# Optimization experiments

Hardware: AMD Instinct MI355X
Metric: run time of the kernel (lower is better)

Reference implementation:

```python
import jax, jax.numpy as jnp
import numpy as np

N_NODES = 50000
N_EDGES = 800000
D = 128        # input_dim == output_dim
D_EDGE = 64    # edge_attr_size
Z_DIM = 2 * D + D_EDGE  # 320


def setup_inputs() -> dict:
    key = jax.random.key(0)
    k1, k2, k3, k4, k5 = jax.random.split(key, 5)
    x = jax.random.normal(k1, (N_NODES, D), dtype=jnp.float32)
    edge_index = jax.random.randint(k2, (2, N_EDGES), 0, N_NODES, dtype=jnp.int64)
    edge_attr = jax.random.normal(k3, (N_EDGES, D_EDGE), dtype=jnp.float32)
    scale = 1.0 / np.sqrt(Z_DIM)
    W_f = jax.random.normal(k4, (Z_DIM, D), dtype=jnp.float32) * scale
    W_s = jax.random.normal(k5, (Z_DIM, D), dtype=jnp.float32) * scale
    b_f = jnp.zeros((D,), dtype=jnp.float32)
    b_s = jnp.zeros((D,), dtype=jnp.float32)
    return {"x": x, "edge_index": edge_index, "edge_attr": edge_attr,
            "W_f": W_f, "b_f": b_f, "W_s": W_s, "b_s": b_s}


def reference(x, edge_index, edge_attr, W_f, b_f, W_s, b_s):
    # Dropout(p=0.0) is identity in inference.
    src = edge_index[0]  # j (message source)
    dst = edge_index[1]  # i (message target)
    # z_e = [x_i, x_j, e_ij]  -> [E, 2D + D_edge]
    z = jnp.concatenate([x[dst], x[src], edge_attr], axis=-1)
    # CGConv message: sigmoid(lin_f(z)) * softplus(lin_s(z))
    msg = jax.nn.sigmoid(z @ W_f + b_f) * jax.nn.softplus(z @ W_s + b_s)
    # scatter-add aggregation + residual
    out = jax.ops.segment_sum(msg, dst, num_segments=x.shape[0]) + x
    # use_activation=True -> ReLU
    return jax.nn.relu(out)
```

## Files before the change

kernel.cpp:

```cpp
#include <hip/hip_runtime.h>
#include <hip/hip_bf16.h>

#define E_TOTAL   800000
#define NN        50000
#define DD        128
#define DE        64
#define ZDIM      320
#define KE        192
#define MT        64
#define NBS       196

typedef short bf16x8 __attribute__((ext_vector_type(8)));
typedef float f32x4  __attribute__((ext_vector_type(4)));

__device__ __forceinline__ unsigned short f2bf(float f) {
    union { float f; unsigned int u; } v; v.f = f;
    unsigned int u = v.u;
    return (unsigned short)((u + 0x7fffu + ((u >> 16) & 1u)) >> 16);
}

__device__ __forceinline__ float bf2f(unsigned short h) {
    union { unsigned u; float f; } v; v.u = ((unsigned)h) << 16; return v.f;
}

__device__ __forceinline__ unsigned pkbf2(float a, float b) {
    __hip_bfloat162 h = __float22bfloat162_rn(make_float2(a, b));
    unsigned u; __builtin_memcpy(&u, &h, 4); return u;
}

__device__ __forceinline__ uint2 pkbf4(float4 v) {
    uint2 r; r.x = pkbf2(v.x, v.y); r.y = pkbf2(v.z, v.w); return r;
}

__device__ __forceinline__ float fast_rcp(float x) {
#if __has_builtin(__builtin_amdgcn_rcpf)
    return __builtin_amdgcn_rcpf(x);
#else
    return 1.0f / x;
#endif
}


__global__ void scan_part(const int* __restrict__ counts, int* __restrict__ partial) {
    __shared__ int red[256];
    int t = threadIdx.x, k = blockIdx.x * 256 + t;
    red[t] = (k < NN) ? counts[k] : 0;
    __syncthreads();
    for (int d = 128; d > 0; d >>= 1) {
        if (t < d) red[t] += red[t + d];
        __syncthreads();
    }
    if (t == 0) partial[blockIdx.x] = red[0];
}

__global__ void scan_top(int* __restrict__ partial) {
    __shared__ int s[256];
    int t = threadIdx.x;
    int v = (t < NBS) ? partial[t] : 0;
    s[t] = v; __syncthreads();
    for (int d = 1; d < 256; d <<= 1) {
        int a = (t >= d) ? s[t - d] : 0;
        __syncthreads();
        s[t] += a;
        __syncthreads();
    }
    if (t < NBS) partial[t] = s[t] - v;
}

__global__ void scan_final(const int* __restrict__ counts,
                           const int* __restrict__ partial,
                           int* __restrict__ cursor) {
    __shared__ int s[256];
    int t = threadIdx.x, k = blockIdx.x * 256 + t;
    int v = (k < NN) ? counts[k] : 0;
    s[t] = v; __syncthreads();
    for (int d = 1; d < 256; d <<= 1) {
        int a = (t >= d) ? s[t - d] : 0;
        __syncthreads();
        s[t] += a;
        __syncthreads();
    }
    if (k < NN) cursor[k] = partial[blockIdx.x] + s[t] - v;
}

__global__ void scatter_kernel(const int* __restrict__ ei, int* __restrict__ cursor,
                               uint2* __restrict__ spak2) {
    int e = blockIdx.x * 256 + threadIdx.x;
    if (e < E_TOTAL) {
        int d = ei[E_TOTAL + e];
        int pos = atomicAdd(&cursor[d], 1);
        uint2 p; p.x = ((unsigned)d << 16) | (unsigned)ei[e]; p.y = (unsigned)e;
        spak2[pos] = p;
    }
}


__global__ void prep_kernel2(const float* __restrict__ x,
                             const int* __restrict__ ei,
                             const float* __restrict__ W_f,
                             const float* __restrict__ W_s,
                             unsigned short* __restrict__ WtE,
                             unsigned short* __restrict__ WtN,
                             int* __restrict__ counts,
                             float* __restrict__ out) {
    int id = blockIdx.x * 256 + threadIdx.x;
    ((float4*)out)[id] = ((const float4*)x)[id];
    if (id < E_TOTAL) atomicAdd(&counts[ei[E_TOTAL + id]], 1);
    if (id < 256 * DE) {
        int n = id >> 6, k = id & 63;
        int ok = 2 * DD + k;
        float wv = (n < DD) ? W_f[ok * DD + n] : W_s[ok * DD + (n - DD)];
        WtE[id] = f2bf(wv);
    } else if (id < 256 * DE + 2 * 256 * DD) {
        int id2 = id - 256 * DE;
        int part = id2 >> 15;
        int r = id2 & 32767;
        int n = r >> 7, k = r & 127;
        int ok = part * DD + k;
        float wv = (n < DD) ? W_f[ok * DD + n] : W_s[ok * DD + (n - DD)];
        WtN[id2] = f2bf(wv);
    }
}

__global__ __launch_bounds__(256, 4)
void node_kernel2(const float* __restrict__ x,
                  const unsigned short* __restrict__ WtN,
                  const float* __restrict__ bf_, const float* __restrict__ bs_,
                  unsigned short* __restrict__ nodeP) {
    __shared__ unsigned short A_lds[MT * DD];
    const int t = threadIdx.x;
    const int m_off = blockIdx.x * MT;
    const int lane = t & 63, w = t >> 6, l15 = lane & 15, quad = lane >> 4;

    #pragma unroll
    for (int it = 0; it < 8; ++it) {
        int idx = it * 256 + t;
        int e = idx >> 5, kq = idx & 31;
        int row = m_off + e; if (row >= NN) row = NN - 1;
        float4 v = ((const float4*)(x + (size_t)row * DD))[kq];
        int g = kq >> 1;
        int col = ((g & ~7) | ((g & 7) ^ (e & 7))) * 8 + (kq & 1) * 4;
        *((uint2*)&A_lds[e * DD + col]) = pkbf4(v);
    }

    const int c0 = 32 * w + l15, c1 = c0 + 16;
    const float bfc0 = bf_[c0], bsc0 = bs_[c0];
    const float bfc1 = bf_[c1], bsc1 = bs_[c1];
    const int nt0 = 2 * w;
    __syncthreads();

    #pragma unroll 1
    for (int part = 0; part < 2; ++part) {
        f32x4 acc[4][4] = {};
        const unsigned short* Bp[4];
        #pragma unroll
        for (int u = 0; u < 4; ++u) {
            int nt = nt0 + ((u < 2) ? u : (6 + u));
            Bp[u] = WtN + (size_t)part * (256 * DD) +
                    (size_t)(nt * 16 + l15) * DD + quad * 8;
        }

        #pragma unroll
        for (int ks = 0; ks < 4; ++ks) {
            bf16x8 af[4], bfr[4];
            #pragma unroll
            for (int i = 0; i < 4; ++i) {
                int m = i * 16 + l15;
                int g = 4 * ks + quad;
                int col = ((g & ~7) | ((g & 7) ^ (l15 & 7))) * 8;
                af[i] = *((const bf16x8*)&A_lds[m * DD + col]);
            }
            #pragma unroll
            for (int u = 0; u < 4; ++u)
                bfr[u] = *((const bf16x8*)(Bp[u] + ks * 32));
            #pragma unroll
            for (int i = 0; i < 4; ++i)
                #pragma unroll
                for (int u = 0; u < 4; ++u)
                    acc[i][u] = __builtin_amdgcn_mfma_f32_16x16x32_bf16(
                        af[i], bfr[u], acc[i][u], 0, 0, 0);
        }

        const float bf0 = part ? 0.f : bfc0, bs0 = part ? 0.f : bsc0;
        const float bf1 = part ? 0.f : bfc1, bs1 = part ? 0.f : bsc1;
        #pragma unroll
        for (int i = 0; i < 4; ++i)
            #pragma unroll
            for (int j = 0; j < 4; ++j) {
                int e = i * 16 + quad * 4 + j;
                int row = m_off + e;
                if (row < NN) {
                    uint2 pk;
                    pk.x = pkbf2(acc[i][0][j] + bf0, acc[i][1][j] + bf1);
                    pk.y = pkbf2(acc[i][2][j] + bs0, acc[i][3][j] + bs1);
                    *((uint2*)(nodeP + (size_t)row * 512 + part * 256 +
                               w * 64 + l15 * 4)) = pk;
                }
            }
    }
}

__global__ __launch_bounds__(256, 3)
void edge_kernel2(const float* __restrict__ ea,
                  const unsigned short* __restrict__ WtE,
                  const unsigned short* __restrict__ nodeP,
                  float* __restrict__ out,
                  const uint2* __restrict__ spak2) {
    __shared__ unsigned short A_lds[MT * DE];
    __shared__ int dst_lds[MT];
    __shared__ int src_lds[MT];
    __shared__ int eid_lds[MT];

    const int t = threadIdx.x;
    const int m_off = blockIdx.x * MT;
    const int lane = t & 63, w = t >> 6, l15 = lane & 15, quad = lane >> 4;

    if (t < MT) {
        uint2 p = spak2[m_off + t];
        dst_lds[t] = (int)(p.x >> 16);
        src_lds[t] = (int)(p.x & 0xffffu);
        eid_lds[t] = (int)p.y;
    }
    __syncthreads();

    const int c0 = 32 * w + l15, c1 = c0 + 16;
    const int np_off = w * 64 + l15 * 4;
    const unsigned short* npS = nodeP + 256 + np_off;

    float4 va[4];
    #pragma unroll
    for (int it = 0; it < 4; ++it) {
        int idx = it * 256 + t;
        int e = idx >> 4;
        va[it] = ((const float4*)(ea + (size_t)eid_lds[e] * DE))[idx & 15];
    }
    uint2 ps[16], pd[4];
    #pragma unroll
    for (int i = 0; i < 4; ++i) {
        #pragma unroll
        for (int j = 0; j < 4; ++j)
            ps[i * 4 + j] = *((const uint2*)(npS +
                (size_t)src_lds[i * 16 + quad * 4 + j] * 512));
        pd[i] = *((const uint2*)(nodeP +
                (size_t)dst_lds[i * 16 + quad * 4] * 512 + np_off));
    }
    #pragma unroll
    for (int it = 0; it < 4; ++it) {
        int idx = it * 256 + t;
        int e = idx >> 4, kq = idx & 15;
        int g = kq >> 1;
        int col = ((g & 7) ^ (e & 7)) * 8 + (kq & 1) * 4;
        *((uint2*)&A_lds[e * DE + col]) = pkbf4(va[it]);
    }

    f32x4 acc[4][4] = {};
    const int nt0 = 2 * w;
    const unsigned short* Bp[4];
    #pragma unroll
    for (int u = 0; u < 4; ++u) {
        int nt = nt0 + ((u < 2) ? u : (6 + u));
        Bp[u] = WtE + (size_t)(nt * 16 + l15) * DE + quad * 8;
    }
    __syncthreads();

    #pragma unroll
    for (int ks = 0; ks < 2; ++ks) {
        bf16x8 af[4], bfr[4];
        #pragma unroll
        for (int i = 0; i < 4; ++i) {
            int m = i * 16 + l15;
            int g = 4 * ks + quad;
            int col = ((g & 7) ^ (l15 & 7)) * 8;
            af[i] = *((const bf16x8*)&A_lds[m * DE + col]);
        }
        #pragma unroll
        for (int u = 0; u < 4; ++u)
            bfr[u] = *((const bf16x8*)(Bp[u] + ks * 32));
        #pragma unroll
        for (int i = 0; i < 4; ++i)
            #pragma unroll
            for (int u = 0; u < 4; ++u)
                acc[i][u] = __builtin_amdgcn_mfma_f32_16x16x32_bf16(
                    af[i], bfr[u], acc[i][u], 0, 0, 0);
    }

    int d = -1;
    float s0 = 0.f, s1 = 0.f, nf0 = 0.f, ns0 = 0.f, nf1 = 0.f, ns1 = 0.f;
    #pragma unroll
    for (int i = 0; i < 4; ++i)
        #pragma unroll
        for (int j = 0; j < 4; ++j) {
            int e = i * 16 + quad * 4 + j;
            int dd = dst_lds[e];
            if (dd != d) {
                if (d >= 0) {
                    atomicAdd(out + (size_t)d * DD + c0, s0);
                    atomicAdd(out + (size_t)d * DD + c1, s1);
                }
                d = dd; s0 = 0.f; s1 = 0.f;
                uint2 pk;
                if (j == 0) pk = pd[i];
                else pk = *((const uint2*)(nodeP + (size_t)dd * 512 + np_off));
                nf0 = bf2f((unsigned short)(pk.x & 0xffffu));
                nf1 = bf2f((unsigned short)(pk.x >> 16));
                ns0 = bf2f((unsigned short)(pk.y & 0xffffu));
                ns1 = bf2f((unsigned short)(pk.y >> 16));
            }
            uint2 pp = ps[i * 4 + j];
            float f0  = acc[i][0][j] + nf0 + bf2f((unsigned short)(pp.x & 0xffffu));
            float f1  = acc[i][1][j] + nf1 + bf2f((unsigned short)(pp.x >> 16));
            float sg0 = acc[i][2][j] + ns0 + bf2f((unsigned short)(pp.y & 0xffffu));
            float sg1 = acc[i][3][j] + ns1 + bf2f((unsigned short)(pp.y >> 16));
            s0 += fast_rcp(1.f + __expf(-f0)) *
                  (fmaxf(sg0, 0.f) + __logf(1.f + __expf(-fabsf(sg0))));
            s1 += fast_rcp(1.f + __expf(-f1)) *
                  (fmaxf(sg1, 0.f) + __logf(1.f + __expf(-fabsf(sg1))));
        }
    atomicAdd(out + (size_t)d * DD + c0, s0);
    atomicAdd(out + (size_t)d * DD + c1, s1);
}


__global__ void prep_kernel(const float* __restrict__ x,
                            const int* __restrict__ ei,
                            const float* __restrict__ W_f,
                            const float* __restrict__ W_s,
                            unsigned short* __restrict__ WtE,
                            unsigned short* __restrict__ WtN,
                            int* __restrict__ counts,
                            float* __restrict__ out) {
    int id = blockIdx.x * 256 + threadIdx.x;
    ((float4*)out)[id] = ((const float4*)x)[id];
    if (id < E_TOTAL) atomicAdd(&counts[ei[E_TOTAL + id]], 1);
    if (id < 256 * KE) {
        int n = id / KE, k = id - n * KE;
        int ok = 128 + k;
        float wv = (n < DD) ? W_f[ok * DD + n] : W_s[ok * DD + (n - DD)];
        WtE[id] = f2bf(wv);
    } else if (id < 256 * KE + 256 * DD) {
        int id2 = id - 256 * KE;
        int n = id2 / DD, k = id2 - n * DD;
        float wv = (n < DD) ? W_f[k * DD + n] : W_s[k * DD + (n - DD)];
        WtN[id2] = f2bf(wv);
    }
}

__global__ __launch_bounds__(256, 4)
void node_kernel(const float* __restrict__ x,
                 const unsigned short* __restrict__ WtN,
                 const float* __restrict__ bf_, const float* __restrict__ bs_,
                 unsigned short* __restrict__ nodeP) {
    __shared__ unsigned short A_lds[MT * DD];
    const int t = threadIdx.x;
    const int m_off = blockIdx.x * MT;
    const int lane = t & 63, w = t >> 6, l15 = lane & 15, quad = lane >> 4;

    #pragma unroll
    for (int it = 0; it < 8; ++it) {
        int idx = it * 256 + t;
        int e = idx >> 5, kq = idx & 31;
        int row = m_off + e; if (row >= NN) row = NN - 1;
        float4 v = ((const float4*)(x + (size_t)row * DD))[kq];
        int g = kq >> 1;
        int col = ((g & ~7) | ((g & 7) ^ (e & 7))) * 8 + (kq & 1) * 4;
        *((uint2*)&A_lds[e * DD + col]) = pkbf4(v);
    }

    f32x4 acc[4][4] = {};
    const int nt0 = 2 * w;
    const unsigned short* Bp[4];
    #pragma unroll
    for (int u = 0; u < 4; ++u) {
        int nt = nt0 + ((u < 2) ? u : (6 + u));
        Bp[u] = WtN + (size_t)(nt * 16 + l15) * DD + quad * 8;
    }
    __syncthreads();

    #pragma unroll
    for (int ks = 0; ks < 4; ++ks) {
        bf16x8 af[4], bfr[4];
        #pragma unroll
        for (int i = 0; i < 4; ++i) {
            int m = i * 16 + l15;
            int g = 4 * ks + quad;
            int col = ((g & ~7) | ((g & 7) ^ (l15 & 7))) * 8;
            af[i] = *((const bf16x8*)&A_lds[m * DD + col]);
        }
        #pragma unroll
        for (int u = 0; u < 4; ++u)
            bfr[u] = *((const bf16x8*)(Bp[u] + ks * 32));
        #pragma unroll
        for (int i = 0; i < 4; ++i)
            #pragma unroll
            for (int u = 0; u < 4; ++u)
                acc[i][u] = __builtin_amdgcn_mfma_f32_16x16x32_bf16(
                    af[i], bfr[u], acc[i][u], 0, 0, 0);
    }

    const int c0 = 32 * w + l15, c1 = c0 + 16;
    const float bf0 = bf_[c0], bs0 = bs_[c0], bf1 = bf_[c1], bs1 = bs_[c1];
    #pragma unroll
    for (int i = 0; i < 4; ++i)
        #pragma unroll
        for (int j = 0; j < 4; ++j) {
            int e = i * 16 + quad * 4 + j;
            int row = m_off + e;
            if (row < NN) {
                uint2 pk;
                pk.x = pkbf2(acc[i][0][j] + bf0, acc[i][1][j] + bf1);
                pk.y = pkbf2(acc[i][2][j] + bs0, acc[i][3][j] + bs1);
                *((uint2*)(nodeP + (size_t)row * 256 + w * 64 + l15 * 4)) = pk;
            }
        }
}

__global__ __launch_bounds__(256, 4)
void edge_kernel(const float* __restrict__ x,
                 const float* __restrict__ ea,
                 const unsigned short* __restrict__ WtE,
                 const unsigned short* __restrict__ nodeP,
                 float* __restrict__ out,
                 const uint2* __restrict__ spak2) {
    __shared__ unsigned short A_lds[MT * KE];
    __shared__ int dst_lds[MT];
    __shared__ int src_lds[MT];
    __shared__ int eid_lds[MT];

    const int t = threadIdx.x;
    const int m_off = blockIdx.x * MT;
    const int lane = t & 63, w = t >> 6, l15 = lane & 15, quad = lane >> 4;

    if (t < MT) {
        uint2 p = spak2[m_off + t];
        dst_lds[t] = (int)(p.x >> 16);
        src_lds[t] = (int)(p.x & 0xffffu);
        eid_lds[t] = (int)p.y;
    }
    __syncthreads();

    #pragma unroll
    for (int it = 0; it < 4; ++it) {
        int idx = it * 256 + t;
        int e = idx >> 4, kq = idx & 15;
        float4 v = ((const float4*)(ea + (size_t)eid_lds[e] * DE))[kq];
        int g = 16 + (kq >> 1);
        int col = ((g & ~7) | ((g & 7) ^ (e & 7))) * 8 + (kq & 1) * 4;
        *((uint2*)&A_lds[e * KE + col]) = pkbf4(v);
    }
    #pragma unroll
    for (int it = 0; it < 8; ++it) {
        int idx = it * 256 + t;
        int e = idx >> 5, kq = idx & 31;
        float4 v = ((const float4*)(x + (size_t)src_lds[e] * DD))[kq];
        int g = kq >> 1;
        int col = ((g & ~7) | ((g & 7) ^ (e & 7))) * 8 + (kq & 1) * 4;
        *((uint2*)&A_lds[e * KE + col]) = pkbf4(v);
    }

    f32x4 acc[4][4] = {};
    const int nt0 = 2 * w;
    const unsigned short* Bp[4];
    #pragma unroll
    for (int u = 0; u < 4; ++u) {
        int nt = nt0 + ((u < 2) ? u : (6 + u));
        Bp[u] = WtE + (size_t)(nt * 16 + l15) * KE + quad * 8;
    }
    __syncthreads();

    #pragma unroll
    for (int ks = 0; ks < 6; ++ks) {
        bf16x8 af[4], bfr[4];
        #pragma unroll
        for (int i = 0; i < 4; ++i) {
            int m = i * 16 + l15;
            int g = 4 * ks + quad;
            int col = ((g & ~7) | ((g & 7) ^ (l15 & 7))) * 8;
            af[i] = *((const bf16x8*)&A_lds[m * KE + col]);
        }
        #pragma unroll
        for (int u = 0; u < 4; ++u)
            bfr[u] = *((const bf16x8*)(Bp[u] + ks * 32));
        #pragma unroll
        for (int i = 0; i < 4; ++i)
            #pragma unroll
            for (int u = 0; u < 4; ++u)
                acc[i][u] = __builtin_amdgcn_mfma_f32_16x16x32_bf16(
                    af[i], bfr[u], acc[i][u], 0, 0, 0);
    }

    const int c0 = 32 * w + l15, c1 = c0 + 16;
    const int np_off = w * 64 + l15 * 4;

    int d = -1;
    float s0 = 0.f, s1 = 0.f, nf0 = 0.f, ns0 = 0.f, nf1 = 0.f, ns1 = 0.f;
    #pragma unroll
    for (int i = 0; i < 4; ++i)
        #pragma unroll
        for (int j = 0; j < 4; ++j) {
            int e = i * 16 + quad * 4 + j;
            int dd = dst_lds[e];
            if (dd != d) {
                if (d >= 0) {
                    atomicAdd(out + (size_t)d * DD + c0, s0);
                    atomicAdd(out + (size_t)d * DD + c1, s1);
                }
                d = dd; s0 = 0.f; s1 = 0.f;
                uint2 pk = *((const uint2*)(nodeP + (size_t)d * 256 + np_off));
                nf0 = bf2f((unsigned short)(pk.x & 0xffffu));
                nf1 = bf2f((unsigned short)(pk.x >> 16));
                ns0 = bf2f((unsigned short)(pk.y & 0xffffu));
                ns1 = bf2f((unsigned short)(pk.y >> 16));
            }
            float f0  = acc[i][0][j] + nf0;
            float sg0 = acc[i][2][j] + ns0;
            s0 += fast_rcp(1.f + __expf(-f0)) *
                  (fmaxf(sg0, 0.f) + __logf(1.f + __expf(-fabsf(sg0))));
            float f1  = acc[i][1][j] + nf1;
            float sg1 = acc[i][3][j] + ns1;
            s1 += fast_rcp(1.f + __expf(-f1)) *
                  (fmaxf(sg1, 0.f) + __logf(1.f + __expf(-fabsf(sg1))));
        }
    atomicAdd(out + (size_t)d * DD + c0, s0);
    atomicAdd(out + (size_t)d * DD + c1, s1);
}

__global__ void relu_kernel(float* __restrict__ out) {
    int id = blockIdx.x * 256 + threadIdx.x;
    if (id < NN * DD / 4) {
        float4 v = ((float4*)out)[id];
        v.x = fmaxf(v.x, 0.0f); v.y = fmaxf(v.y, 0.0f);
        v.z = fmaxf(v.z, 0.0f); v.w = fmaxf(v.w, 0.0f);
        ((float4*)out)[id] = v;
    }
}


__global__ void prep_fb(const float* __restrict__ x,
                        const float* __restrict__ W_f,
                        const float* __restrict__ W_s,
                        unsigned short* __restrict__ Wt,
                        float* __restrict__ out) {
    int id = blockIdx.x * 256 + threadIdx.x;
    if (id < NN * DD / 4)
        ((float4*)out)[id] = ((const float4*)x)[id];
    if (id < 2 * DD * ZDIM) {
        int n = id / ZDIM, k = id - n * ZDIM;
        float wv = (n < DD) ? W_f[k * DD + n] : W_s[k * DD + (n - DD)];
        Wt[n * ZDIM + k] = f2bf(wv);
    }
}

__global__ __launch_bounds__(256, 3)
void edge_fb(const float* __restrict__ x,
             const int* __restrict__ ei,
             const float* __restrict__ ea,
             const unsigned short* __restrict__ Wt,
             const float* __restrict__ bf_,
             const float* __restrict__ bs_,
             float* __restrict__ out) {
    __shared__ unsigned short A_lds[MT * ZDIM];
    __shared__ int dst_lds[MT];
    __shared__ int src_lds[MT];

    const int t = threadIdx.x;
    const int m_off = blockIdx.x * MT;
    const int lane = t & 63, w = t >> 6, l15 = lane & 15, quad = lane >> 4;

    if (t < MT) dst_lds[t] = ei[E_TOTAL + m_off + t];
    else if (t < 2 * MT) src_lds[t - MT] = ei[m_off + (t - MT)];
    __syncthreads();

    #pragma unroll
    for (int it = 0; it < 4; ++it) {
        int idx = it * 256 + t;
        int e = idx >> 4, kq = idx & 15;
        float4 v = ((const float4*)(ea + (size_t)(m_off + e) * DE))[kq];
        int g = 32 + (kq >> 1);
        int col = ((g & ~7) | ((g & 7) ^ (e & 7))) * 8 + (kq & 1) * 4;
        *((uint2*)&A_lds[e * ZDIM + col]) = pkbf4(v);
    }
    #pragma unroll
    for (int it = 0; it < 8; ++it) {
        int idx = it * 256 + t;
        int e = idx >> 5, kq = idx & 31;
        float4 v = ((const float4*)(x + (size_t)dst_lds[e] * DD))[kq];
        int g = kq >> 1;
        int col = ((g & ~7) | ((g & 7) ^ (e & 7))) * 8 + (kq & 1) * 4;
        *((uint2*)&A_lds[e * ZDIM + col]) = pkbf4(v);
    }
    #pragma unroll
    for (int it = 0; it < 8; ++it) {
        int idx = it * 256 + t;
        int e = idx >> 5, kq = idx & 31;
        float4 v = ((const float4*)(x + (size_t)src_lds[e] * DD))[kq];
        int g = 16 + (kq >> 1);
        int col = ((g & ~7) | ((g & 7) ^ (e & 7))) * 8 + (kq & 1) * 4;
        *((uint2*)&A_lds[e * ZDIM + col]) = pkbf4(v);
    }

    f32x4 acc[4][4] = {};
    const int nt0 = 2 * w;
    const unsigned short* Bp[4];
    #pragma unroll
    for (int u = 0; u < 4; ++u) {
        int nt = nt0 + ((u < 2) ? u : (6 + u));
        Bp[u] = Wt + (size_t)(nt * 16 + l15) * ZDIM + quad * 8;
    }
    __syncthreads();

    #pragma unroll
    for (int ks = 0; ks < 10; ++ks) {
        bf16x8 af[4], bfr[4];
        #pragma unroll
        for (int i = 0; i < 4; ++i) {
            int m = i * 16 + l15;
            int g = 4 * ks + quad;
            int col = ((g & ~7) | ((g & 7) ^ (l15 & 7))) * 8;
            af[i] = *((const bf16x8*)&A_lds[m * ZDIM + col]);
        }
        #pragma unroll
        for (int u = 0; u < 4; ++u)
            bfr[u] = *((const bf16x8*)(Bp[u] + ks * 32));
        #pragma unroll
        for (int i = 0; i < 4; ++i)
            #pragma unroll
            for (int u = 0; u < 4; ++u)
                acc[i][u] = __builtin_amdgcn_mfma_f32_16x16x32_bf16(
                    af[i], bfr[u], acc[i][u], 0, 0, 0);
    }

    const int c0 = 32 * w + l15, c1 = c0 + 16;
    const float bf0 = bf_[c0], bs0 = bs_[c0], bf1 = bf_[c1], bs1 = bs_[c1];
    #pragma unroll
    for (int i = 0; i < 4; ++i)
        #pragma unroll
        for (int j = 0; j < 4; ++j) {
            int e = i * 16 + quad * 4 + j;
            float* op = out + (size_t)dst_lds[e] * DD;
            float f0 = acc[i][0][j] + bf0;
            float sg0 = acc[i][2][j] + bs0;
            atomicAdd(op + c0, fast_rcp(1.f + __expf(-f0)) *
                (fmaxf(sg0, 0.f) + __logf(1.f + __expf(-fabsf(sg0)))));
            float f1 = acc[i][1][j] + bf1;
            float sg1 = acc[i][3][j] + bs1;
            atomicAdd(op + c1, fast_rcp(1.f + __expf(-f1)) *
                (fmaxf(sg1, 0.f) + __logf(1.f + __expf(-fabsf(sg1)))));
        }
}


extern "C" void kernel_launch(void* const* d_in, const int* in_sizes, int n_in,
                              void* d_out, int out_size, void* d_ws, size_t ws_size,
                              hipStream_t stream) {
    (void)in_sizes; (void)n_in; (void)out_size;
    const float* x   = (const float*)d_in[0];
    const int*   ei  = (const int*)d_in[1];
    const float* ea  = (const float*)d_in[2];
    const float* W_f = (const float*)d_in[3];
    const float* b_f = (const float*)d_in[4];
    const float* W_s = (const float*)d_in[5];
    const float* b_s = (const float*)d_in[6];
    float* out = (float*)d_out;

    char* ws = (char*)d_ws;
    const size_t WS_NEED2 = 58164864;
    const size_t WS_NEED1 = 32564864;

    if (ws_size >= WS_NEED2) {
        unsigned short* WtE2   = (unsigned short*)ws;
        unsigned short* WtN2   = (unsigned short*)(ws + 32768);
        int*            counts = (int*)(ws + 163840);
        int*            cursor = (int*)(ws + 363840);
        int*            partial= (int*)(ws + 563840);
        uint2*          spak2  = (uint2*)(ws + 564864);
        unsigned short* nodeP  = (unsigned short*)(ws + 6964864);

        hipMemsetAsync(counts, 0, NN * sizeof(int), stream);
        prep_kernel2<<<NN * DD / 4 / 256, 256, 0, stream>>>(
            x, ei, W_f, W_s, WtE2, WtN2, counts, out);
        scan_part<<<NBS, 256, 0, stream>>>(counts, partial);
        scan_top<<<1, 256, 0, stream>>>(partial);
        scan_final<<<NBS, 256, 0, stream>>>(counts, partial, cursor);
        scatter_kernel<<<(E_TOTAL + 255) / 256, 256, 0, stream>>>(ei, cursor, spak2);
        node_kernel2<<<(NN + MT - 1) / MT, 256, 0, stream>>>(x, WtN2, b_f, b_s, nodeP);
        edge_kernel2<<<E_TOTAL / MT, 256, 0, stream>>>(
            ea, WtE2, nodeP, out, spak2);
    } else if (ws_size >= WS_NEED1) {
        unsigned short* WtE    = (unsigned short*)ws;
        unsigned short* WtN    = (unsigned short*)(ws + 98304);
        int*            counts = (int*)(ws + 163840);
        int*            cursor = (int*)(ws + 363840);
        int*            partial= (int*)(ws + 563840);
        uint2*          spak2  = (uint2*)(ws + 564864);
        unsigned short* nodeP  = (unsigned short*)(ws + 6964864);

        hipMemsetAsync(counts, 0, NN * sizeof(int), stream);
        prep_kernel<<<NN * DD / 4 / 256, 256, 0, stream>>>(
            x, ei, W_f, W_s, WtE, WtN, counts, out);
        scan_part<<<NBS, 256, 0, stream>>>(counts, partial);
        scan_top<<<1, 256, 0, stream>>>(partial);
        scan_final<<<NBS, 256, 0, stream>>>(counts, partial, cursor);
        scatter_kernel<<<(E_TOTAL + 255) / 256, 256, 0, stream>>>(ei, cursor, spak2);
        node_kernel<<<(NN + MT - 1) / MT, 256, 0, stream>>>(x, WtN, b_f, b_s, nodeP);
        edge_kernel<<<E_TOTAL / MT, 256, 0, stream>>>(
            x, ea, WtE, nodeP, out, spak2);
    } else {
        unsigned short* Wt = (unsigned short*)ws;
        prep_fb<<<6250, 256, 0, stream>>>(x, W_f, W_s, Wt, out);
        edge_fb<<<E_TOTAL / MT, 256, 0, stream>>>(x, ei, ea, Wt, b_f, b_s, out);
    }

    relu_kernel<<<6250, 256, 0, stream>>>(out);
}
```

Before: 671.9 us.

## Split node GEMM parts across grid and widen edge kernel to 512 threads

The node projection kernel now launches a 2D grid so each block computes only one of the two weight parts, rather than looping over both. The nodeP layout changes to interleave each column's f and s values into one 32-bit word. The edge kernel moves to 512 threads per block, with each thread owning one output column instead of two, which cuts per-thread registers and gathers. The aim is more parallelism and occupancy, at the cost of narrower 4-byte gathers per thread and re-staging x into LDS twice in the node kernel.

```diff
diff --git a/kernel.cpp b/kernel.cpp
--- a/kernel.cpp
+++ b/kernel.cpp
@@ -126,10 +126,11 @@
 void node_kernel2(const float* __restrict__ x,
                   const unsigned short* __restrict__ WtN,
                   const float* __restrict__ bf_, const float* __restrict__ bs_,
-                  unsigned short* __restrict__ nodeP) {
+                  unsigned int* __restrict__ nodeP32) {
     __shared__ unsigned short A_lds[MT * DD];
     const int t = threadIdx.x;
     const int m_off = blockIdx.x * MT;
+    const int part = blockIdx.y;
     const int lane = t & 63, w = t >> 6, l15 = lane & 15, quad = lane >> 4;
 
     #pragma unroll
@@ -143,67 +144,59 @@
         *((uint2*)&A_lds[e * DD + col]) = pkbf4(v);
     }
 
-    const int c0 = 32 * w + l15, c1 = c0 + 16;
-    const float bfc0 = bf_[c0], bsc0 = bs_[c0];
-    const float bfc1 = bf_[c1], bsc1 = bs_[c1];
+    f32x4 acc[4][4] = {};
     const int nt0 = 2 * w;
-    __syncthreads();
-
-    #pragma unroll 1
-    for (int part = 0; part < 2; ++part) {
-        f32x4 acc[4][4] = {};
-        const unsigned short* Bp[4];
-        #pragma unroll
-        for (int u = 0; u < 4; ++u) {
-            int nt = nt0 + ((u < 2) ? u : (6 + u));
-            Bp[u] = WtN + (size_t)part * (256 * DD) +
-                    (size_t)(nt * 16 + l15) * DD + quad * 8;
-        }
-
-        #pragma unroll
-        for (int ks = 0; ks < 4; ++ks) {
-            bf16x8 af[4], bfr[4];
-            #pragma unroll
-            for (int i = 0; i < 4; ++i) {
-                int m = i * 16 + l15;
-                int g = 4 * ks + quad;
-                int col = ((g & ~7) | ((g & 7) ^ (l15 & 7))) * 8;
-                af[i] = *((const bf16x8*)&A_lds[m * DD + col]);
-            }
+    const unsigned short* Bp[4];
+    #pragma unroll
+    for (int u = 0; u < 4; ++u) {
+        int nt = nt0 + ((u < 2) ? u : (6 + u));
+        Bp[u] = WtN + (size_t)part * (256 * DD) +
+                (size_t)(nt * 16 + l15) * DD + quad * 8;
+    }
+    __syncthreads();
+
+    #pragma unroll
+    for (int ks = 0; ks < 4; ++ks) {
+        bf16x8 af[4], bfr[4];
+        #pragma unroll
+        for (int i = 0; i < 4; ++i) {
+            int m = i * 16 + l15;
+            int g = 4 * ks + quad;
+            int col = ((g & ~7) | ((g & 7) ^ (l15 & 7))) * 8;
+            af[i] = *((const bf16x8*)&A_lds[m * DD + col]);
+        }
+        #pragma unroll
+        for (int u = 0; u < 4; ++u)
+            bfr[u] = *((const bf16x8*)(Bp[u] + ks * 32));
+        #pragma unroll
+        for (int i = 0; i < 4; ++i)
             #pragma unroll
             for (int u = 0; u < 4; ++u)
-                bfr[u] = *((const bf16x8*)(Bp[u] + ks * 32));
-            #pragma unroll
-            for (int i = 0; i < 4; ++i)
-                #pragma unroll
-                for (int u = 0; u < 4; ++u)
-                    acc[i][u] = __builtin_amdgcn_mfma_f32_16x16x32_bf16(
-                        af[i], bfr[u], acc[i][u], 0, 0, 0);
-        }
-
-        const float bf0 = part ? 0.f : bfc0, bs0 = part ? 0.f : bsc0;
-        const float bf1 = part ? 0.f : bfc1, bs1 = part ? 0.f : bsc1;
-        #pragma unroll
-        for (int i = 0; i < 4; ++i)
-            #pragma unroll
-            for (int j = 0; j < 4; ++j) {
-                int e = i * 16 + quad * 4 + j;
-                int row = m_off + e;
-                if (row < NN) {
-                    uint2 pk;
-                    pk.x = pkbf2(acc[i][0][j] + bf0, acc[i][1][j] + bf1);
-                    pk.y = pkbf2(acc[i][2][j] + bs0, acc[i][3][j] + bs1);
-                    *((uint2*)(nodeP + (size_t)row * 512 + part * 256 +
-                               w * 64 + l15 * 4)) = pk;
-                }
+                acc[i][u] = __builtin_amdgcn_mfma_f32_16x16x32_bf16(
+                    af[i], bfr[u], acc[i][u], 0, 0, 0);
+    }
+
+    const int c0 = 32 * w + l15, c1 = c0 + 16;
+    const float bf0 = part ? 0.f : bf_[c0], bs0 = part ? 0.f : bs_[c0];
+    const float bf1 = part ? 0.f : bf_[c1], bs1 = part ? 0.f : bs_[c1];
+    #pragma unroll
+    for (int i = 0; i < 4; ++i)
+        #pragma unroll
+        for (int j = 0; j < 4; ++j) {
+            int e = i * 16 + quad * 4 + j;
+            int row = m_off + e;
+            if (row < NN) {
+                unsigned int* np = nodeP32 + (size_t)row * 256 + part * 128;
+                np[c0] = pkbf2(acc[i][0][j] + bf0, acc[i][2][j] + bs0);
+                np[c1] = pkbf2(acc[i][1][j] + bf1, acc[i][3][j] + bs1);
             }
-    }
-}
-
-__global__ __launch_bounds__(256, 3)
+        }
+}
+
+__global__ __launch_bounds__(512, 4)
 void edge_kernel2(const float* __restrict__ ea,
                   const unsigned short* __restrict__ WtE,
-                  const unsigned short* __restrict__ nodeP,
+                  const unsigned int* __restrict__ nodeP32,
                   float* __restrict__ out,
                   const uint2* __restrict__ spak2) {
     __shared__ unsigned short A_lds[MT * DE];
@@ -213,7 +206,7 @@
 
     const int t = threadIdx.x;
     const int m_off = blockIdx.x * MT;
-    const int lane = t & 63, w = t >> 6, l15 = lane & 15, quad = lane >> 4;
+    const int lane = t & 63, w2 = t >> 6, l15 = lane & 15, quad = lane >> 4;
 
     if (t < MT) {
         uint2 p = spak2[m_off + t];
@@ -223,49 +216,45 @@
     }
     __syncthreads();
 
-    const int c0 = 32 * w + l15, c1 = c0 + 16;
-    const int np_off = w * 64 + l15 * 4;
-    const unsigned short* npS = nodeP + 256 + np_off;
-
-    float4 va[4];
-    #pragma unroll
-    for (int it = 0; it < 4; ++it) {
-        int idx = it * 256 + t;
+    const int c = 16 * w2 + l15;
+
+    float4 va[2];
+    #pragma unroll
+    for (int it = 0; it < 2; ++it) {
+        int idx = it * 512 + t;
         int e = idx >> 4;
         va[it] = ((const float4*)(ea + (size_t)eid_lds[e] * DE))[idx & 15];
     }
-    uint2 ps[16], pd[4];
+    unsigned int ps[16], pd[4];
     #pragma unroll
     for (int i = 0; i < 4; ++i) {
         #pragma unroll
         for (int j = 0; j < 4; ++j)
-            ps[i * 4 + j] = *((const uint2*)(npS +
-                (size_t)src_lds[i * 16 + quad * 4 + j] * 512));
-        pd[i] = *((const uint2*)(nodeP +
-                (size_t)dst_lds[i * 16 + quad * 4] * 512 + np_off));
-    }
-    #pragma unroll
-    for (int it = 0; it < 4; ++it) {
-        int idx = it * 256 + t;
+            ps[i * 4 + j] = nodeP32[(size_t)src_lds[i * 16 + quad * 4 + j] * 256
+                                    + 128 + c];
+        pd[i] = nodeP32[(size_t)dst_lds[i * 16 + quad * 4] * 256 + c];
+    }
+    #pragma unroll
+    for (int it = 0; it < 2; ++it) {
+        int idx = it * 512 + t;
         int e = idx >> 4, kq = idx & 15;
         int g = kq >> 1;
         int col = ((g & 7) ^ (e & 7)) * 8 + (kq & 1) * 4;
         *((uint2*)&A_lds[e * DE + col]) = pkbf4(va[it]);
     }
 
-    f32x4 acc[4][4] = {};
-    const int nt0 = 2 * w;
-    const unsigned short* Bp[4];
-    #pragma unroll
-    for (int u = 0; u < 4; ++u) {
-        int nt = nt0 + ((u < 2) ? u : (6 + u));
+    f32x4 acc[4][2] = {};
+    const unsigned short* Bp[2];
+    #pragma unroll
+    for (int u = 0; u < 2; ++u) {
+        int nt = w2 + u * 8;
         Bp[u] = WtE + (size_t)(nt * 16 + l15) * DE + quad * 8;
     }
     __syncthreads();
 
     #pragma unroll
     for (int ks = 0; ks < 2; ++ks) {
-        bf16x8 af[4], bfr[4];
+        bf16x8 af[4], bfr[2];
         #pragma unroll
         for (int i = 0; i < 4; ++i) {
             int m = i * 16 + l15;
@@ -274,18 +263,18 @@
             af[i] = *((const bf16x8*)&A_lds[m * DE + col]);
         }
         #pragma unroll
-        for (int u = 0; u < 4; ++u)
+        for (int u = 0; u < 2; ++u)
             bfr[u] = *((const bf16x8*)(Bp[u] + ks * 32));
         #pragma unroll
         for (int i = 0; i < 4; ++i)
             #pragma unroll
-            for (int u = 0; u < 4; ++u)
+            for (int u = 0; u < 2; ++u)
                 acc[i][u] = __builtin_amdgcn_mfma_f32_16x16x32_bf16(
                     af[i], bfr[u], acc[i][u], 0, 0, 0);
     }
 
     int d = -1;
-    float s0 = 0.f, s1 = 0.f, nf0 = 0.f, ns0 = 0.f, nf1 = 0.f, ns1 = 0.f;
+    float s0 = 0.f, nf = 0.f, ns = 0.f;
     #pragma unroll
     for (int i = 0; i < 4; ++i)
         #pragma unroll
@@ -293,31 +282,22 @@
             int e = i * 16 + quad * 4 + j;
             int dd = dst_lds[e];
             if (dd != d) {
-                if (d >= 0) {
-                    atomicAdd(out + (size_t)d * DD + c0, s0);
-                    atomicAdd(out + (size_t)d * DD + c1, s1);
-                }
-                d = dd; s0 = 0.f; s1 = 0.f;
-                uint2 pk;
+                if (d >= 0)
+                    atomicAdd(out + (size_t)d * DD + c, s0);
+                d = dd; s0 = 0.f;
+                unsigned int pk;
                 if (j == 0) pk = pd[i];
-                else pk = *((const uint2*)(nodeP + (size_t)dd * 512 + np_off));
-                nf0 = bf2f((unsigned short)(pk.x & 0xffffu));
-                nf1 = bf2f((unsigned short)(pk.x >> 16));
-                ns0 = bf2f((unsigned short)(pk.y & 0xffffu));
-                ns1 = bf2f((unsigned short)(pk.y >> 16));
+                else pk = nodeP32[(size_t)dd * 256 + c];
+                nf = bf2f((unsigned short)(pk & 0xffffu));
+                ns = bf2f((unsigned short)(pk >> 16));
             }
-            uint2 pp = ps[i * 4 + j];
-            float f0  = acc[i][0][j] + nf0 + bf2f((unsigned short)(pp.x & 0xffffu));
-            float f1  = acc[i][1][j] + nf1 + bf2f((unsigned short)(pp.x >> 16));
-            float sg0 = acc[i][2][j] + ns0 + bf2f((unsigned short)(pp.y & 0xffffu));
-            float sg1 = acc[i][3][j] + ns1 + bf2f((unsigned short)(pp.y >> 16));
-            s0 += fast_rcp(1.f + __expf(-f0)) *
-                  (fmaxf(sg0, 0.f) + __logf(1.f + __expf(-fabsf(sg0))));
-            s1 += fast_rcp(1.f + __expf(-f1)) *
-                  (fmaxf(sg1, 0.f) + __logf(1.f + __expf(-fabsf(sg1))));
-        }
-    atomicAdd(out + (size_t)d * DD + c0, s0);
-    atomicAdd(out + (size_t)d * DD + c1, s1);
+            unsigned int pp = ps[i * 4 + j];
+            float f  = acc[i][0][j] + nf + bf2f((unsigned short)(pp & 0xffffu));
+            float sg = acc[i][1][j] + ns + bf2f((unsigned short)(pp >> 16));
+            s0 += fast_rcp(1.f + __expf(-f)) *
+                  (fmaxf(sg, 0.f) + __logf(1.f + __expf(-fabsf(sg))));
+        }
+    atomicAdd(out + (size_t)d * DD + c, s0);
 }
 
 
@@ -673,7 +653,7 @@
         int*            cursor = (int*)(ws + 363840);
         int*            partial= (int*)(ws + 563840);
         uint2*          spak2  = (uint2*)(ws + 564864);
-        unsigned short* nodeP  = (unsigned short*)(ws + 6964864);
+        unsigned int*   nodeP32= (unsigned int*)(ws + 6964864);
 
         hipMemsetAsync(counts, 0, NN * sizeof(int), stream);
         prep_kernel2<<<NN * DD / 4 / 256, 256, 0, stream>>>(
@@ -682,9 +662,10 @@
         scan_top<<<1, 256, 0, stream>>>(partial);
         scan_final<<<NBS, 256, 0, stream>>>(counts, partial, cursor);
         scatter_kernel<<<(E_TOTAL + 255) / 256, 256, 0, stream>>>(ei, cursor, spak2);
-        node_kernel2<<<(NN + MT - 1) / MT, 256, 0, stream>>>(x, WtN2, b_f, b_s, nodeP);
-        edge_kernel2<<<E_TOTAL / MT, 256, 0, stream>>>(
-            ea, WtE2, nodeP, out, spak2);
+        dim3 ng((NN + MT - 1) / MT, 2);
+        node_kernel2<<<ng, 256, 0, stream>>>(x, WtN2, b_f, b_s, nodeP32);
+        edge_kernel2<<<E_TOTAL / MT, 512, 0, stream>>>(
+            ea, WtE2, nodeP32, out, spak2);
     } else if (ws_size >= WS_NEED1) {
         unsigned short* WtE    = (unsigned short*)ws;
         unsigned short* WtN    = (unsigned short*)(ws + 98304);
```

After: 635.0 us. 1.06x faster.
